# Kernel tuning notes

Hardware: AMD Instinct MI355X
Metric: run time of the kernel (lower is better)

The kernel has to match this reference:

```python
import jax, jax.numpy as jnp
import numpy as np

N = 500_000
CHANNELS = 256
NUM_GRAPHS = 2048


def setup_inputs() -> dict:
    key = jax.random.key(0)
    k1, k2, k3 = jax.random.split(key, 3)
    features = jax.random.normal(k1, (N, CHANNELS), dtype=jnp.float32)
    batch = jnp.sort(jax.random.randint(k2, (N,), 0, NUM_GRAPHS, dtype=jnp.int64))
    batch = batch.at[-1].set(NUM_GRAPHS - 1)  # pin max so num_segments == NUM_GRAPHS
    W_att = jax.random.normal(k3, (CHANNELS, 1), dtype=jnp.float32) * (1.0 / np.sqrt(CHANNELS))
    b_att = jnp.zeros((1,), dtype=jnp.float32)
    return {"features": features, "batch": batch, "W_att": W_att, "b_att": b_att}


def reference(features, batch, W_att, b_att):
    # attention: Linear(channels, 1) -> Sigmoid, per node  [N, 1]
    weights = jax.nn.sigmoid(features @ W_att + b_att)
    # weighted per-graph sum: equivalent to the python loop over batch ids,
    # fused as a single segment reduction. num_segments = batch.max()+1 = NUM_GRAPHS.
    weighted = features * weights  # [N, C]
    out = jax.ops.segment_sum(weighted, batch, num_segments=NUM_GRAPHS)  # [B, C]
    return out
```

## Files before the change

kernel.cpp:

```cpp
#include <hip/hip_runtime.h>


constexpr int kChannels     = 256;
constexpr int kNodesPerWave = 64;

__global__ void hgp_fused_kernel(const float* __restrict__ features,
                                 const int*   __restrict__ batch,
                                 const float* __restrict__ W_att,
                                 const float* __restrict__ b_att,
                                 float*       __restrict__ out,
                                 int n_nodes) {
    const int gtid = blockIdx.x * blockDim.x + threadIdx.x;
    const int wave = gtid >> 6;
    const int lane = threadIdx.x & 63;

    const int start = wave * kNodesPerWave;
    if (start >= n_nodes) return;
    const int end = min(start + kNodesPerWave, n_nodes);

    const float4 w4  = reinterpret_cast<const float4*>(W_att)[lane];
    const float bias = b_att[0];

    const float4* __restrict__ frow = reinterpret_cast<const float4*>(features);

    float4 acc = make_float4(0.f, 0.f, 0.f, 0.f);
    int cur_seg = batch[start];

    float4 cur = frow[(size_t)start * (kChannels / 4) + lane];
    int seg = cur_seg;

    for (int n = start; n < end; ++n) {
        float4 nxt  = make_float4(0.f, 0.f, 0.f, 0.f);
        int    nseg = cur_seg;
        if (n + 1 < end) {
            nxt  = frow[(size_t)(n + 1) * (kChannels / 4) + lane];
            nseg = batch[n + 1];
        }

        if (seg != cur_seg) {
            float* o = out + (size_t)cur_seg * kChannels + lane * 4;
            atomicAdd(o + 0, acc.x);
            atomicAdd(o + 1, acc.y);
            atomicAdd(o + 2, acc.z);
            atomicAdd(o + 3, acc.w);
            acc = make_float4(0.f, 0.f, 0.f, 0.f);
            cur_seg = seg;
        }

        float p = cur.x * w4.x + cur.y * w4.y + cur.z * w4.z + cur.w * w4.w;
        #pragma unroll
        for (int off = 32; off > 0; off >>= 1) p += __shfl_xor(p, off, 64);

        const float wgt = 1.0f / (1.0f + __expf(-(p + bias)));

        acc.x += cur.x * wgt;
        acc.y += cur.y * wgt;
        acc.z += cur.z * wgt;
        acc.w += cur.w * wgt;

        cur = nxt;
        seg = nseg;
    }

    float* o = out + (size_t)cur_seg * kChannels + lane * 4;
    atomicAdd(o + 0, acc.x);
    atomicAdd(o + 1, acc.y);
    atomicAdd(o + 2, acc.z);
    atomicAdd(o + 3, acc.w);
}

extern "C" void kernel_launch(void* const* d_in, const int* in_sizes, int n_in,
                              void* d_out, int out_size, void* d_ws, size_t ws_size,
                              hipStream_t stream) {
    const float* features = (const float*)d_in[0];
    const int*   batch    = (const int*)d_in[1];
    const float* W_att    = (const float*)d_in[2];
    const float* b_att    = (const float*)d_in[3];
    float*       out      = (float*)d_out;

    const int n_nodes = in_sizes[1];

    hipMemsetAsync(d_out, 0, (size_t)out_size * sizeof(float), stream);

    const int num_waves       = (n_nodes + kNodesPerWave - 1) / kNodesPerWave;
    const int waves_per_block = 4;
    const int blocks          = (num_waves + waves_per_block - 1) / waves_per_block;

    hgp_fused_kernel<<<blocks, 256, 0, stream>>>(features, batch, W_att, b_att, out, n_nodes);
}
```

Measured before the change: 671.9 us.

## Assign one block per graph via binary search, drop atomics and memset

Each block now handles one graph: it binary-searches the sorted batch array for the segment bounds, splits the segment across four waves, and combines the partial sums in LDS before one plain store. This removes the output memset, the global float atomics and the per-node batch loads. Each wave also processes four rows per iteration with nontemporal loads to raise memory-level parallelism. The risk is load imbalance, since there are only 2048 blocks with about 244 rows each, plus the binary-search latency at block start.

```diff
diff --git a/kernel.cpp b/kernel.cpp
--- a/kernel.cpp
+++ b/kernel.cpp
@@ -1,72 +1,98 @@
 #include <hip/hip_runtime.h>
 
 
-constexpr int kChannels     = 256;
-constexpr int kNodesPerWave = 64;
+constexpr int kChannels  = 256;
+constexpr int kVecPerRow = kChannels / 4;
 
-__global__ void hgp_fused_kernel(const float* __restrict__ features,
-                                 const int*   __restrict__ batch,
-                                 const float* __restrict__ W_att,
-                                 const float* __restrict__ b_att,
-                                 float*       __restrict__ out,
-                                 int n_nodes) {
-    const int gtid = blockIdx.x * blockDim.x + threadIdx.x;
-    const int wave = gtid >> 6;
+typedef float vfloat4 __attribute__((ext_vector_type(4)));
+
+__device__ inline int lower_bound_i32(const int* __restrict__ b, int n, int v) {
+    int lo = 0, hi = n;
+    while (lo < hi) {
+        int mid = (lo + hi) >> 1;
+        if (b[mid] < v) lo = mid + 1; else hi = mid;
+    }
+    return lo;
+}
+
+__device__ inline float sigmoidf(float x) {
+    return 1.0f / (1.0f + __expf(-x));
+}
+
+__global__ void hgp_seg_kernel(const float* __restrict__ features,
+                               const int*   __restrict__ batch,
+                               const float* __restrict__ W_att,
+                               const float* __restrict__ b_att,
+                               float*       __restrict__ out,
+                               int n_nodes) {
+    const int g    = blockIdx.x;
+    const int wv   = threadIdx.x >> 6;
     const int lane = threadIdx.x & 63;
 
-    const int start = wave * kNodesPerWave;
-    if (start >= n_nodes) return;
-    const int end = min(start + kNodesPerWave, n_nodes);
+    const int seg_start = lower_bound_i32(batch, n_nodes, g);
+    const int seg_end   = lower_bound_i32(batch, n_nodes, g + 1);
+    const int seg_len   = seg_end - seg_start;
+
+    const int q   = (seg_len + 3) >> 2;
+    const int ws_ = seg_start + wv * q;
+    const int we_ = min(ws_ + q, seg_end);
 
     const float4 w4  = reinterpret_cast<const float4*>(W_att)[lane];
     const float bias = b_att[0];
+    const vfloat4* __restrict__ frow = reinterpret_cast<const vfloat4*>(features);
 
-    const float4* __restrict__ frow = reinterpret_cast<const float4*>(features);
+    float ax = 0.f, ay = 0.f, az = 0.f, aw = 0.f;
 
-    float4 acc = make_float4(0.f, 0.f, 0.f, 0.f);
-    int cur_seg = batch[start];
+    int n = ws_;
+    for (; n + 4 <= we_; n += 4) {
+        const size_t base = (size_t)n * kVecPerRow + lane;
+        vfloat4 r0 = __builtin_nontemporal_load(&frow[base]);
+        vfloat4 r1 = __builtin_nontemporal_load(&frow[base + 1 * kVecPerRow]);
+        vfloat4 r2 = __builtin_nontemporal_load(&frow[base + 2 * kVecPerRow]);
+        vfloat4 r3 = __builtin_nontemporal_load(&frow[base + 3 * kVecPerRow]);
 
-    float4 cur = frow[(size_t)start * (kChannels / 4) + lane];
-    int seg = cur_seg;
+        float p0 = r0[0] * w4.x + r0[1] * w4.y + r0[2] * w4.z + r0[3] * w4.w;
+        float p1 = r1[0] * w4.x + r1[1] * w4.y + r1[2] * w4.z + r1[3] * w4.w;
+        float p2 = r2[0] * w4.x + r2[1] * w4.y + r2[2] * w4.z + r2[3] * w4.w;
+        float p3 = r3[0] * w4.x + r3[1] * w4.y + r3[2] * w4.z + r3[3] * w4.w;
 
-    for (int n = start; n < end; ++n) {
-        float4 nxt  = make_float4(0.f, 0.f, 0.f, 0.f);
-        int    nseg = cur_seg;
-        if (n + 1 < end) {
-            nxt  = frow[(size_t)(n + 1) * (kChannels / 4) + lane];
-            nseg = batch[n + 1];
+        #pragma unroll
+        for (int off = 32; off > 0; off >>= 1) {
+            p0 += __shfl_xor(p0, off, 64);
+            p1 += __shfl_xor(p1, off, 64);
+            p2 += __shfl_xor(p2, off, 64);
+            p3 += __shfl_xor(p3, off, 64);
         }
 
-        if (seg != cur_seg) {
-            float* o = out + (size_t)cur_seg * kChannels + lane * 4;
-            atomicAdd(o + 0, acc.x);
-            atomicAdd(o + 1, acc.y);
-            atomicAdd(o + 2, acc.z);
-            atomicAdd(o + 3, acc.w);
-            acc = make_float4(0.f, 0.f, 0.f, 0.f);
-            cur_seg = seg;
-        }
+        const float g0 = sigmoidf(p0 + bias);
+        const float g1 = sigmoidf(p1 + bias);
+        const float g2 = sigmoidf(p2 + bias);
+        const float g3 = sigmoidf(p3 + bias);
 
-        float p = cur.x * w4.x + cur.y * w4.y + cur.z * w4.z + cur.w * w4.w;
+        ax += r0[0] * g0 + r1[0] * g1 + r2[0] * g2 + r3[0] * g3;
+        ay += r0[1] * g0 + r1[1] * g1 + r2[1] * g2 + r3[1] * g3;
+        az += r0[2] * g0 + r1[2] * g1 + r2[2] * g2 + r3[2] * g3;
+        aw += r0[3] * g0 + r1[3] * g1 + r2[3] * g2 + r3[3] * g3;
+    }
+    for (; n < we_; ++n) {
+        vfloat4 r = __builtin_nontemporal_load(&frow[(size_t)n * kVecPerRow + lane]);
+        float p = r[0] * w4.x + r[1] * w4.y + r[2] * w4.z + r[3] * w4.w;
         #pragma unroll
         for (int off = 32; off > 0; off >>= 1) p += __shfl_xor(p, off, 64);
-
-        const float wgt = 1.0f / (1.0f + __expf(-(p + bias)));
-
-        acc.x += cur.x * wgt;
-        acc.y += cur.y * wgt;
-        acc.z += cur.z * wgt;
-        acc.w += cur.w * wgt;
-
-        cur = nxt;
-        seg = nseg;
+        const float gg = sigmoidf(p + bias);
+        ax += r[0] * gg; ay += r[1] * gg; az += r[2] * gg; aw += r[3] * gg;
     }
 
-    float* o = out + (size_t)cur_seg * kChannels + lane * 4;
-    atomicAdd(o + 0, acc.x);
-    atomicAdd(o + 1, acc.y);
-    atomicAdd(o + 2, acc.z);
-    atomicAdd(o + 3, acc.w);
+    __shared__ float lds[4][kChannels];
+    lds[wv][lane * 4 + 0] = ax;
+    lds[wv][lane * 4 + 1] = ay;
+    lds[wv][lane * 4 + 2] = az;
+    lds[wv][lane * 4 + 3] = aw;
+    __syncthreads();
+
+    const int t = threadIdx.x;
+    const float s = lds[0][t] + lds[1][t] + lds[2][t] + lds[3][t];
+    out[(size_t)g * kChannels + t] = s;
 }
 
 extern "C" void kernel_launch(void* const* d_in, const int* in_sizes, int n_in,
@@ -78,13 +104,9 @@
     const float* b_att    = (const float*)d_in[3];
     float*       out      = (float*)d_out;
 
-    const int n_nodes = in_sizes[1];
+    const int n_nodes    = in_sizes[1];
+    const int num_graphs = out_size / kChannels;
 
-    hipMemsetAsync(d_out, 0, (size_t)out_size * sizeof(float), stream);
-
-    const int num_waves       = (n_nodes + kNodesPerWave - 1) / kNodesPerWave;
-    const int waves_per_block = 4;
-    const int blocks          = (num_waves + waves_per_block - 1) / waves_per_block;
-
-    hgp_fused_kernel<<<blocks, 256, 0, stream>>>(features, batch, W_att, b_att, out, n_nodes);
+    hgp_seg_kernel<<<num_graphs, 256, 0, stream>>>(features, batch, W_att, b_att,
+                                                   out, n_nodes);
 }
```

Result: faster. 625.9 us (-6.8%).
